# Optimization experiments

Hardware: AMD Instinct MI355X
Metric: run time of the kernel (lower is better)

## Reference

```python
import jax, jax.numpy as jnp
import numpy as np
import math

N_HEADS = 16
D_Q = 1024
D_K = 1024
D_V = 1024
D_OUT = 1024
HID = D_OUT // N_HEADS  # 64
BATCH = 2
SEQ = 2048


def setup_inputs() -> dict:
    key = jax.random.key(0)
    ks = jax.random.split(key, 7)
    stdv = 1.0 / math.sqrt(HID)
    so = 1.0 / math.sqrt(D_OUT)
    return {
        "q": jax.random.normal(ks[0], (BATCH, SEQ, D_Q), dtype=jnp.float32),
        "k": jax.random.normal(ks[1], (BATCH, SEQ, D_K), dtype=jnp.float32),
        "v": jax.random.normal(ks[2], (BATCH, SEQ, D_V), dtype=jnp.float32),
        "W_query": jax.random.uniform(ks[3], (N_HEADS, D_Q, HID), jnp.float32, -stdv, stdv),
        "W_key": jax.random.uniform(ks[4], (N_HEADS, D_K, HID), jnp.float32, -stdv, stdv),
        "W_val": jax.random.uniform(ks[5], (N_HEADS, D_V, HID), jnp.float32, -stdv, stdv),
        "W_out": jax.random.uniform(ks[6], (N_HEADS, HID, D_OUT), jnp.float32, -so, so),
    }


def reference(q, k, v, W_query, W_key, W_val, W_out):
    norm = 1.0 / math.sqrt(HID)
    # per-head projections: [h, b, s, e]
    Q = jnp.einsum("bqd,hde->hbqe", q, W_query)
    K = jnp.einsum("bkd,hde->hbke", k, W_key)
    V = jnp.einsum("bkd,hde->hbke", v, W_val)
    # scaled dot-product attention
    compat = norm * jnp.einsum("hbqe,hbke->hbqk", Q, K)
    attn = jax.nn.softmax(compat, axis=-1)
    heads = jnp.einsum("hbqk,hbke->hbqe", attn, V)
    # output projection: concat heads then W_out == sum over h of per-head proj
    out = jnp.einsum("hbqe,heo->bqo", heads, W_out)
    return out
```

## Files before the change

### kernel.cpp

```cpp
#include <hip/hip_runtime.h>
#include <hip/hip_bf16.h>

typedef __bf16 bf16;
typedef __bf16 bf16x8 __attribute__((ext_vector_type(8)));
typedef __bf16 bf16x4 __attribute__((ext_vector_type(4)));
typedef float  f32x4  __attribute__((ext_vector_type(4)));

#define MFMA16(a,b,c) __builtin_amdgcn_mfma_f32_16x16x32_bf16(a, b, c, 0, 0, 0)

__device__ __forceinline__ void gl2lds16(const bf16* g, bf16* l) {
    __builtin_amdgcn_global_load_lds(
        (__attribute__((address_space(1))) void*)g,
        (__attribute__((address_space(3))) void*)l, 16, 0, 0);
}

__global__ __launch_bounds__(256)
void prep_kernel(const float* __restrict__ q, const float* __restrict__ k,
                 const float* __restrict__ v, const float* __restrict__ Wq,
                 const float* __restrict__ Wk, const float* __restrict__ Wv,
                 const float* __restrict__ Wo, bf16* __restrict__ Xcat,
                 bf16* __restrict__ Wqkv, bf16* __restrict__ Wot)
{
    __shared__ bf16 Tl[64][72];
    const int bid = blockIdx.x;
    const int tid = threadIdx.x;

    if (bid < 6144) {
        int gidx = bid * 256 + tid;
        int t    = gidx >> 19;
        int off  = (gidx & 0x7FFFF) * 8;
        const float* src = (t == 0) ? q : (t == 1) ? k : v;
        const float4 f0 = *(const float4*)&src[off];
        const float4 f1 = *(const float4*)&src[off + 4];
        bf16x8 p = { (bf16)f0.x, (bf16)f0.y, (bf16)f0.z, (bf16)f0.w,
                     (bf16)f1.x, (bf16)f1.y, (bf16)f1.z, (bf16)f1.w };
        *(bf16x8*)&Xcat[(size_t)gidx * 8] = p;
        return;
    }
    if (bid < 6912) {
        int idx = bid - 6144;
        int x = idx & 15, z = idx >> 4;
        int t = z >> 4, h = z & 15;
        const float* inp = ((t == 0) ? Wq : (t == 1) ? Wk : Wv) + (size_t)h * 65536;
        bf16* outp = Wqkv + (size_t)t * 1024 * 1024 + (size_t)h * 65536;
        int r0 = x * 64;
        #pragma unroll
        for (int i = 0; i < 2; i++) {
            int s = tid + i * 256;
            int r = s >> 3, c8 = (s & 7) * 8;
            const float* ap = &inp[(size_t)(r0 + r) * 64 + c8];
            float4 f0 = *(const float4*)ap;
            float4 f1 = *(const float4*)(ap + 4);
            bf16x8 p = { (bf16)f0.x, (bf16)f0.y, (bf16)f0.z, (bf16)f0.w,
                         (bf16)f1.x, (bf16)f1.y, (bf16)f1.z, (bf16)f1.w };
            *(bf16x8*)&Tl[r][c8] = p;
        }
        __syncthreads();
        #pragma unroll
        for (int i = 0; i < 2; i++) {
            int s = tid + i * 256;
            int c = s >> 3, r8 = (s & 7) * 8;
            bf16x8 p;
            #pragma unroll
            for (int j = 0; j < 8; j++) p[j] = Tl[r8 + j][c];
            *(bf16x8*)&outp[(size_t)c * 1024 + r0 + r8] = p;
        }
        return;
    }
    {
        int idx = bid - 6912;
        int y = idx & 15, h = idx >> 4;
        int c0 = y * 64;
        const float* inp = Wo + (size_t)h * 65536;
        bf16* outp = Wot + (size_t)h * 64;
        #pragma unroll
        for (int i = 0; i < 2; i++) {
            int s = tid + i * 256;
            int r = s >> 3, c8 = (s & 7) * 8;
            const float* ap = &inp[(size_t)r * 1024 + c0 + c8];
            float4 f0 = *(const float4*)ap;
            float4 f1 = *(const float4*)(ap + 4);
            bf16x8 p = { (bf16)f0.x, (bf16)f0.y, (bf16)f0.z, (bf16)f0.w,
                         (bf16)f1.x, (bf16)f1.y, (bf16)f1.z, (bf16)f1.w };
            *(bf16x8*)&Tl[r][c8] = p;
        }
        __syncthreads();
        #pragma unroll
        for (int i = 0; i < 2; i++) {
            int s = tid + i * 256;
            int c = s >> 3, r8 = (s & 7) * 8;
            bf16x8 p;
            #pragma unroll
            for (int j = 0; j < 8; j++) p[j] = Tl[r8 + j][c];
            *(bf16x8*)&outp[(size_t)(c0 + c) * 1024 + r8] = p;
        }
    }
}

__global__ __launch_bounds__(256)
void qkv_gemm(const bf16* __restrict__ Xcat, const bf16* __restrict__ Wqkv,
              bf16* __restrict__ Cq, bf16* __restrict__ Ck, bf16* __restrict__ Vt,
              float qscale)
{
    __shared__ bf16 Al[128 * 64];
    __shared__ bf16 Bl[128 * 64];
    const int slab  = blockIdx.x >> 5;
    const int mbase = (blockIdx.x & 31) * 128;
    const int nbase = blockIdx.y * 128;
    const int tid = threadIdx.x;
    const int w = tid >> 6, lane = tid & 63;
    const int lm = lane & 15, q4 = lane >> 4;
    const int wr = (w >> 1) * 64, wc = (w & 1) * 64;
    const int lrow = lane >> 3, lsw = ((lane & 7) ^ lrow) * 8;

    const bf16* A  = Xcat + (size_t)slab * 4096 * 1024;
    const bf16* Bt = Wqkv + (size_t)slab * 1024 * 1024;

    f32x4 acc[4][4] = {};

    for (int k0 = 0; k0 < 1024; k0 += 64) {
        __syncthreads();
        #pragma unroll
        for (int i = 0; i < 4; i++) {
            int c = w * 4 + i;
            gl2lds16(&A [(size_t)(mbase + c * 8 + lrow) * 1024 + k0 + lsw], &Al[c * 512]);
            gl2lds16(&Bt[(size_t)(nbase + c * 8 + lrow) * 1024 + k0 + lsw], &Bl[c * 512]);
        }
        __syncthreads();
        #pragma unroll
        for (int kk2 = 0; kk2 < 2; kk2++) {
            bf16x8 a[4], bfr[4];
            const int g = ((kk2 * 4 + q4) ^ (lm & 7)) * 8;
            #pragma unroll
            for (int i = 0; i < 4; i++) a[i]   = *(const bf16x8*)&Al[(wr + i * 16 + lm) * 64 + g];
            #pragma unroll
            for (int j = 0; j < 4; j++) bfr[j] = *(const bf16x8*)&Bl[(wc + j * 16 + lm) * 64 + g];
            #pragma unroll
            for (int i = 0; i < 4; i++)
                #pragma unroll
                for (int j = 0; j < 4; j++)
                    acc[i][j] = MFMA16(a[i], bfr[j], acc[i][j]);
        }
    }

    if (slab == 2) {
        #pragma unroll
        for (int i = 0; i < 4; i++)
            #pragma unroll
            for (int j = 0; j < 4; j++) {
                int s0  = mbase + wr + i * 16 + q4 * 4;
                int col = nbase + wc + j * 16 + lm;
                int sp  = (s0 & ~31) | (((s0 >> 2) & 3) * 8) | (((s0 >> 4) & 1) * 4);
                bf16x4 p = { (bf16)acc[i][j][0], (bf16)acc[i][j][1],
                             (bf16)acc[i][j][2], (bf16)acc[i][j][3] };
                *(bf16x4*)&Vt[(size_t)col * 4096 + sp] = p;
            }
    } else {
        bf16* C = (slab == 0) ? Cq : Ck;
        const float scale = (slab == 0) ? qscale : 1.0f;
        #pragma unroll
        for (int i = 0; i < 4; i++)
            #pragma unroll
            for (int j = 0; j < 4; j++)
                #pragma unroll
                for (int r = 0; r < 4; r++) {
                    int row = mbase + wr + i * 16 + q4 * 4 + r;
                    int col = nbase + wc + j * 16 + lm;
                    C[(size_t)row * 1024 + col] = (bf16)(acc[i][j][r] * scale);
                }
    }
}

__global__ __launch_bounds__(256)
void outproj_gemm(const bf16* __restrict__ A, const bf16* __restrict__ Bt,
                  float* __restrict__ C)
{
    __shared__ bf16 Al[64 * 64];
    __shared__ bf16 Bl[128 * 64];
    const int mbase = blockIdx.x * 64;
    const int nbase = blockIdx.y * 128;
    const int tid = threadIdx.x;
    const int w = tid >> 6, lane = tid & 63;
    const int lm = lane & 15, q4 = lane >> 4;
    const int wm = (w >> 1) * 32, wn = (w & 1) * 64;
    const int lrow = lane >> 3, lsw = ((lane & 7) ^ lrow) * 8;

    f32x4 acc[2][4] = {};

    for (int k0 = 0; k0 < 1024; k0 += 64) {
        __syncthreads();
        #pragma unroll
        for (int i = 0; i < 2; i++) {
            int c = w * 2 + i;
            gl2lds16(&A[(size_t)(mbase + c * 8 + lrow) * 1024 + k0 + lsw], &Al[c * 512]);
        }
        #pragma unroll
        for (int i = 0; i < 4; i++) {
            int c = w * 4 + i;
            gl2lds16(&Bt[(size_t)(nbase + c * 8 + lrow) * 1024 + k0 + lsw], &Bl[c * 512]);
        }
        __syncthreads();
        #pragma unroll
        for (int kk2 = 0; kk2 < 2; kk2++) {
            bf16x8 a[2], bfr[4];
            const int g = ((kk2 * 4 + q4) ^ (lm & 7)) * 8;
            #pragma unroll
            for (int i = 0; i < 2; i++) a[i]   = *(const bf16x8*)&Al[(wm + i * 16 + lm) * 64 + g];
            #pragma unroll
            for (int j = 0; j < 4; j++) bfr[j] = *(const bf16x8*)&Bl[(wn + j * 16 + lm) * 64 + g];
            #pragma unroll
            for (int i = 0; i < 2; i++)
                #pragma unroll
                for (int j = 0; j < 4; j++)
                    acc[i][j] = MFMA16(a[i], bfr[j], acc[i][j]);
        }
    }

    #pragma unroll
    for (int i = 0; i < 2; i++)
        #pragma unroll
        for (int j = 0; j < 4; j++)
            #pragma unroll
            for (int r = 0; r < 4; r++) {
                int row = mbase + wm + i * 16 + q4 * 4 + r;
                int col = nbase + wn + j * 16 + lm;
                C[(size_t)row * 1024 + col] = acc[i][j][r];
            }
}

__global__ __launch_bounds__(256)
void attn_kernel(const bf16* __restrict__ Qp, const bf16* __restrict__ Kp,
                 const bf16* __restrict__ Vt, bf16* __restrict__ Hd)
{
    __shared__ bf16 Kl[2][64 * 64];
    __shared__ bf16 Vl[2][64 * 64];

    const int qt = blockIdx.x, b = blockIdx.y, h = blockIdx.z;
    const int qbase = qt * 128;
    const int tid  = threadIdx.x;
    const int w    = tid >> 6, lane = tid & 63;
    const int lm   = lane & 15, q4 = lane >> 4;
    const int lrow = lane >> 3, lsw = ((lane & 7) ^ lrow) * 8;

    const bf16* Qh = Qp + (size_t)(b * 2048 + qbase + w * 32) * 1024 + h * 64;
    const bf16* Kh = Kp + (size_t)(b * 2048) * 1024 + h * 64;
    const bf16* Vh = Vt + (size_t)(h * 64) * 4096 + b * 2048;

    bf16x8 Qf[2][2];
    #pragma unroll
    for (int i = 0; i < 2; i++)
        #pragma unroll
        for (int kk2 = 0; kk2 < 2; kk2++)
            Qf[i][kk2] = *(const bf16x8*)&Qh[(size_t)(i * 16 + lm) * 1024 + kk2 * 32 + q4 * 8];

    f32x4 O[2][4] = {};
    float lsum[2] = {};

    auto stage = [&](int kt, int d) {
        #pragma unroll
        for (int i = 0; i < 2; i++) {
            int c = w * 2 + i;
            gl2lds16(&Kh[(size_t)(kt * 64 + c * 8 + lrow) * 1024 + lsw], &Kl[d][c * 512]);
            gl2lds16(&Vh[(size_t)(c * 8 + lrow) * 4096 + kt * 64 + lsw], &Vl[d][c * 512]);
        }
    };

    stage(0, 0);

    for (int kt = 0; kt < 32; kt++) {
        __syncthreads();
        if (kt < 31) stage(kt + 1, (kt + 1) & 1);
        const bf16* Kd = &Kl[kt & 1][0];
        const bf16* Vd = &Vl[kt & 1][0];

        f32x4 St[2][4] = {};
        #pragma unroll
        for (int ctp = 0; ctp < 4; ctp++) {
            #pragma unroll
            for (int kk2 = 0; kk2 < 2; kk2++) {
                const int g = ((kk2 * 4 + q4) ^ (lm & 7)) * 8;
                bf16x8 kf = *(const bf16x8*)&Kd[(ctp * 16 + lm) * 64 + g];
                #pragma unroll
                for (int i = 0; i < 2; i++)
                    St[i][ctp] = MFMA16(kf, Qf[i][kk2], St[i][ctp]);
            }
        }

        #pragma unroll
        for (int kk4 = 0; kk4 < 2; kk4++) {
            bf16x8 Pf[2];
            #pragma unroll
            for (int i = 0; i < 2; i++)
                #pragma unroll
                for (int j = 0; j < 8; j++) {
                    float p = __builtin_amdgcn_exp2f(St[i][kk4 * 2 + (j >> 2)][j & 3]);
                    lsum[i] += p;
                    Pf[i][j] = (bf16)p;
                }
            #pragma unroll
            for (int et = 0; et < 4; et++) {
                const int g = ((kk4 * 4 + q4) ^ (lm & 7)) * 8;
                bf16x8 vf = *(const bf16x8*)&Vd[(et * 16 + lm) * 64 + g];
                #pragma unroll
                for (int i = 0; i < 2; i++)
                    O[i][et] = MFMA16(Pf[i], vf, O[i][et]);
            }
        }
    }

    float rl[2][4];
    #pragma unroll
    for (int i = 0; i < 2; i++) {
        float l = lsum[i];
        l += __shfl_xor(l, 16, 64);
        l += __shfl_xor(l, 32, 64);
        #pragma unroll
        for (int r = 0; r < 4; r++) {
            float lr = __shfl(l, (lane & 48) + ((lane >> 4) & 3) * 4 + r, 64);
            rl[i][r] = 1.0f / lr;
        }
    }

    #pragma unroll
    for (int i = 0; i < 2; i++)
        #pragma unroll
        for (int et = 0; et < 4; et++)
            #pragma unroll
            for (int r = 0; r < 4; r++) {
                int row = b * 2048 + qbase + w * 32 + i * 16 + q4 * 4 + r;
                Hd[(size_t)row * 1024 + h * 64 + et * 16 + lm] =
                    (bf16)(O[i][et][r] * rl[i][r]);
            }
}

extern "C" void kernel_launch(void* const* d_in, const int* in_sizes, int n_in,
                              void* d_out, int out_size, void* d_ws, size_t ws_size,
                              hipStream_t stream)
{
    const float* q  = (const float*)d_in[0];
    const float* k  = (const float*)d_in[1];
    const float* v  = (const float*)d_in[2];
    const float* Wq = (const float*)d_in[3];
    const float* Wk = (const float*)d_in[4];
    const float* Wv = (const float*)d_in[5];
    const float* Wo = (const float*)d_in[6];
    float* out = (float*)d_out;

    const size_t Mi = 1024 * 1024;
    bf16* Xcat  = (bf16*)d_ws;
    bf16* Hd    = Xcat;
    bf16* Wqkv  = Xcat + 12 * Mi;
    bf16* Wot   = Xcat + 15 * Mi;
    bf16* Qproj = Xcat + 16 * Mi;
    bf16* Kproj = Xcat + 20 * Mi;
    bf16* Vtb   = (bf16*)d_out;

    const float qscale = 0.125f * 1.4426950408889634f;

    prep_kernel<<<7168, 256, 0, stream>>>(q, k, v, Wq, Wk, Wv, Wo, Xcat, Wqkv, Wot);
    qkv_gemm<<<dim3(96, 8), 256, 0, stream>>>(Xcat, Wqkv, Qproj, Kproj, Vtb, qscale);
    attn_kernel<<<dim3(16, 2, 16), 256, 0, stream>>>(Qproj, Kproj, Vtb, Hd);
    outproj_gemm<<<dim3(64, 8), 256, 0, stream>>>(Hd, Wot, out);
}
```

Baseline: 216.1 us.

## Halve attention query tile, compute row sums via MFMA, add wave priority hints

```diff
diff --git a/kernel.cpp b/kernel.cpp
--- a/kernel.cpp
+++ b/kernel.cpp
@@ -236,25 +236,26 @@
     __shared__ bf16 Vl[2][64 * 64];
 
     const int qt = blockIdx.x, b = blockIdx.y, h = blockIdx.z;
-    const int qbase = qt * 128;
+    const int qbase = qt * 64;
     const int tid  = threadIdx.x;
     const int w    = tid >> 6, lane = tid & 63;
     const int lm   = lane & 15, q4 = lane >> 4;
     const int lrow = lane >> 3, lsw = ((lane & 7) ^ lrow) * 8;
 
-    const bf16* Qh = Qp + (size_t)(b * 2048 + qbase + w * 32) * 1024 + h * 64;
+    const bf16* Qh = Qp + (size_t)(b * 2048 + qbase + w * 16) * 1024 + h * 64;
     const bf16* Kh = Kp + (size_t)(b * 2048) * 1024 + h * 64;
     const bf16* Vh = Vt + (size_t)(h * 64) * 4096 + b * 2048;
 
-    bf16x8 Qf[2][2];
+    bf16x8 Qf[2];
     #pragma unroll
-    for (int i = 0; i < 2; i++)
-        #pragma unroll
-        for (int kk2 = 0; kk2 < 2; kk2++)
-            Qf[i][kk2] = *(const bf16x8*)&Qh[(size_t)(i * 16 + lm) * 1024 + kk2 * 32 + q4 * 8];
-
-    f32x4 O[2][4] = {};
-    float lsum[2] = {};
+    for (int kk2 = 0; kk2 < 2; kk2++)
+        Qf[kk2] = *(const bf16x8*)&Qh[(size_t)lm * 1024 + kk2 * 32 + q4 * 8];
+
+    const bf16 one = (bf16)1.0f;
+    const bf16x8 ones = { one, one, one, one, one, one, one, one };
+
+    f32x4 O[4] = {};
+    f32x4 Lacc = {};
 
     auto stage = [&](int kt, int d) {
         #pragma unroll
@@ -273,64 +274,49 @@
         const bf16* Kd = &Kl[kt & 1][0];
         const bf16* Vd = &Vl[kt & 1][0];
 
-        f32x4 St[2][4] = {};
+        f32x4 St[4] = {};
+        __builtin_amdgcn_s_setprio(1);
         #pragma unroll
         for (int ctp = 0; ctp < 4; ctp++) {
             #pragma unroll
             for (int kk2 = 0; kk2 < 2; kk2++) {
                 const int g = ((kk2 * 4 + q4) ^ (lm & 7)) * 8;
                 bf16x8 kf = *(const bf16x8*)&Kd[(ctp * 16 + lm) * 64 + g];
-                #pragma unroll
-                for (int i = 0; i < 2; i++)
-                    St[i][ctp] = MFMA16(kf, Qf[i][kk2], St[i][ctp]);
+                St[ctp] = MFMA16(kf, Qf[kk2], St[ctp]);
             }
         }
+        __builtin_amdgcn_s_setprio(0);
 
         #pragma unroll
         for (int kk4 = 0; kk4 < 2; kk4++) {
-            bf16x8 Pf[2];
-            #pragma unroll
-            for (int i = 0; i < 2; i++)
-                #pragma unroll
-                for (int j = 0; j < 8; j++) {
-                    float p = __builtin_amdgcn_exp2f(St[i][kk4 * 2 + (j >> 2)][j & 3]);
-                    lsum[i] += p;
-                    Pf[i][j] = (bf16)p;
-                }
+            bf16x8 Pf;
+            #pragma unroll
+            for (int j = 0; j < 8; j++)
+                Pf[j] = (bf16)__builtin_amdgcn_exp2f(St[kk4 * 2 + (j >> 2)][j & 3]);
+            __builtin_amdgcn_s_setprio(1);
+            Lacc = MFMA16(Pf, ones, Lacc);
             #pragma unroll
             for (int et = 0; et < 4; et++) {
                 const int g = ((kk4 * 4 + q4) ^ (lm & 7)) * 8;
                 bf16x8 vf = *(const bf16x8*)&Vd[(et * 16 + lm) * 64 + g];
-                #pragma unroll
-                for (int i = 0; i < 2; i++)
-                    O[i][et] = MFMA16(Pf[i], vf, O[i][et]);
+                O[et] = MFMA16(Pf, vf, O[et]);
             }
-        }
-    }
-
-    float rl[2][4];
+            __builtin_amdgcn_s_setprio(0);
+        }
+    }
+
+    float rl[4];
     #pragma unroll
-    for (int i = 0; i < 2; i++) {
-        float l = lsum[i];
-        l += __shfl_xor(l, 16, 64);
-        l += __shfl_xor(l, 32, 64);
+    for (int r = 0; r < 4; r++) rl[r] = 1.0f / Lacc[r];
+
+    #pragma unroll
+    for (int et = 0; et < 4; et++)
         #pragma unroll
         for (int r = 0; r < 4; r++) {
-            float lr = __shfl(l, (lane & 48) + ((lane >> 4) & 3) * 4 + r, 64);
-            rl[i][r] = 1.0f / lr;
-        }
-    }
-
-    #pragma unroll
-    for (int i = 0; i < 2; i++)
-        #pragma unroll
-        for (int et = 0; et < 4; et++)
-            #pragma unroll
-            for (int r = 0; r < 4; r++) {
-                int row = b * 2048 + qbase + w * 32 + i * 16 + q4 * 4 + r;
-                Hd[(size_t)row * 1024 + h * 64 + et * 16 + lm] =
-                    (bf16)(O[i][et][r] * rl[i][r]);
-            }
+            int row = b * 2048 + qbase + w * 16 + q4 * 4 + r;
+            Hd[(size_t)row * 1024 + h * 64 + et * 16 + lm] =
+                (bf16)(O[et][r] * rl[r]);
+        }
 }
 
 extern "C" void kernel_launch(void* const* d_in, const int* in_sizes, int n_in,
@@ -359,6 +345,6 @@
 
     prep_kernel<<<7168, 256, 0, stream>>>(q, k, v, Wq, Wk, Wv, Wo, Xcat, Wqkv, Wot);
     qkv_gemm<<<dim3(96, 8), 256, 0, stream>>>(Xcat, Wqkv, Qproj, Kproj, Vtb, qscale);
-    attn_kernel<<<dim3(16, 2, 16), 256, 0, stream>>>(Qproj, Kproj, Vtb, Hd);
+    attn_kernel<<<dim3(32, 2, 16), 256, 0, stream>>>(Qproj, Kproj, Vtb, Hd);
     outproj_gemm<<<dim3(64, 8), 256, 0, stream>>>(Hd, Wot, out);
 }
```

After: 220.5 us. 2.0% more time.

## Split attention KV tiles across warp pairs and double grid size

Applied to the files above, without the earlier changes.

```diff
diff --git a/kernel.cpp b/kernel.cpp
--- a/kernel.cpp
+++ b/kernel.cpp
@@ -228,7 +228,7 @@
             }
 }
 
-__global__ __launch_bounds__(256)
+__global__ __launch_bounds__(256, 4)
 void attn_kernel(const bf16* __restrict__ Qp, const bf16* __restrict__ Kp,
                  const bf16* __restrict__ Vt, bf16* __restrict__ Hd)
 {
@@ -236,13 +236,15 @@
     __shared__ bf16 Vl[2][64 * 64];
 
     const int qt = blockIdx.x, b = blockIdx.y, h = blockIdx.z;
-    const int qbase = qt * 128;
+    const int qbase = qt * 64;
     const int tid  = threadIdx.x;
     const int w    = tid >> 6, lane = tid & 63;
+    const int p    = w & 1;
+    const int kvh  = w >> 1;
     const int lm   = lane & 15, q4 = lane >> 4;
     const int lrow = lane >> 3, lsw = ((lane & 7) ^ lrow) * 8;
 
-    const bf16* Qh = Qp + (size_t)(b * 2048 + qbase + w * 32) * 1024 + h * 64;
+    const bf16* Qh = Qp + (size_t)(b * 2048 + qbase + p * 32) * 1024 + h * 64;
     const bf16* Kh = Kp + (size_t)(b * 2048) * 1024 + h * 64;
     const bf16* Vh = Vt + (size_t)(h * 64) * 4096 + b * 2048;
 
@@ -253,8 +255,11 @@
         for (int kk2 = 0; kk2 < 2; kk2++)
             Qf[i][kk2] = *(const bf16x8*)&Qh[(size_t)(i * 16 + lm) * 1024 + kk2 * 32 + q4 * 8];
 
+    const bf16 one = (bf16)1.0f;
+    const bf16x8 ones = { one, one, one, one, one, one, one, one };
+
     f32x4 O[2][4] = {};
-    float lsum[2] = {};
+    f32x4 Lacc[2] = {};
 
     auto stage = [&](int kt, int d) {
         #pragma unroll
@@ -265,72 +270,91 @@
         }
     };
 
-    stage(0, 0);
-
-    for (int kt = 0; kt < 32; kt++) {
-        __syncthreads();
-        if (kt < 31) stage(kt + 1, (kt + 1) & 1);
-        const bf16* Kd = &Kl[kt & 1][0];
-        const bf16* Vd = &Vl[kt & 1][0];
-
-        f32x4 St[2][4] = {};
-        #pragma unroll
-        for (int ctp = 0; ctp < 4; ctp++) {
+    const int phase = (qt * 3 + h * 5 + b * 16) & 31;
+
+    stage(phase, 0);
+
+    for (int it = 0; it < 32; it++) {
+        __syncthreads();
+        if (it < 31) stage((it + 1 + phase) & 31, (it + 1) & 1);
+        const bf16* Kd = &Kl[it & 1][0];
+        const bf16* Vd = &Vl[it & 1][0];
+
+        f32x4 St[2][2] = {};
+        __builtin_amdgcn_s_setprio(1);
+        #pragma unroll
+        for (int c2 = 0; c2 < 2; c2++) {
+            const int ctp = kvh * 2 + c2;
             #pragma unroll
             for (int kk2 = 0; kk2 < 2; kk2++) {
                 const int g = ((kk2 * 4 + q4) ^ (lm & 7)) * 8;
                 bf16x8 kf = *(const bf16x8*)&Kd[(ctp * 16 + lm) * 64 + g];
                 #pragma unroll
                 for (int i = 0; i < 2; i++)
-                    St[i][ctp] = MFMA16(kf, Qf[i][kk2], St[i][ctp]);
+                    St[i][c2] = MFMA16(kf, Qf[i][kk2], St[i][c2]);
             }
         }
-
-        #pragma unroll
-        for (int kk4 = 0; kk4 < 2; kk4++) {
-            bf16x8 Pf[2];
+        __builtin_amdgcn_s_setprio(0);
+
+        bf16x8 Pf[2];
+        #pragma unroll
+        for (int i = 0; i < 2; i++)
+            #pragma unroll
+            for (int j = 0; j < 8; j++)
+                Pf[i][j] = (bf16)__builtin_amdgcn_exp2f(St[i][j >> 2][j & 3]);
+
+        __builtin_amdgcn_s_setprio(1);
+        #pragma unroll
+        for (int i = 0; i < 2; i++) Lacc[i] = MFMA16(Pf[i], ones, Lacc[i]);
+        const int gv = ((kvh * 4 + q4) ^ (lm & 7)) * 8;
+        #pragma unroll
+        for (int et = 0; et < 4; et++) {
+            bf16x8 vf = *(const bf16x8*)&Vd[(et * 16 + lm) * 64 + gv];
             #pragma unroll
             for (int i = 0; i < 2; i++)
-                #pragma unroll
-                for (int j = 0; j < 8; j++) {
-                    float p = __builtin_amdgcn_exp2f(St[i][kk4 * 2 + (j >> 2)][j & 3]);
-                    lsum[i] += p;
-                    Pf[i][j] = (bf16)p;
+                O[i][et] = MFMA16(Pf[i], vf, O[i][et]);
+        }
+        __builtin_amdgcn_s_setprio(0);
+    }
+
+    __syncthreads();
+    float* Ol = (float*)&Kl[0][0];
+    float* Ll = (float*)&Vl[0][0];
+    if (kvh == 1) {
+        #pragma unroll
+        for (int i = 0; i < 2; i++)
+            #pragma unroll
+            for (int et = 0; et < 4; et++)
+                #pragma unroll
+                for (int r = 0; r < 4; r++)
+                    Ol[p * 2048 + (i * 16 + q4 * 4 + r) * 64 + et * 16 + lm] = O[i][et][r];
+        if (lm == 0) {
+            #pragma unroll
+            for (int i = 0; i < 2; i++)
+                #pragma unroll
+                for (int r = 0; r < 4; r++)
+                    Ll[p * 32 + i * 16 + q4 * 4 + r] = Lacc[i][r];
+        }
+    }
+    __syncthreads();
+    if (kvh == 0) {
+        #pragma unroll
+        for (int i = 0; i < 2; i++) {
+            float rl[4];
+            #pragma unroll
+            for (int r = 0; r < 4; r++)
+                rl[r] = 1.0f / (Lacc[i][r] + Ll[p * 32 + i * 16 + q4 * 4 + r]);
+            #pragma unroll
+            for (int et = 0; et < 4; et++)
+                #pragma unroll
+                for (int r = 0; r < 4; r++) {
+                    float o = O[i][et][r] +
+                              Ol[p * 2048 + (i * 16 + q4 * 4 + r) * 64 + et * 16 + lm];
+                    int row = b * 2048 + qbase + p * 32 + i * 16 + q4 * 4 + r;
+                    Hd[(size_t)row * 1024 + h * 64 + et * 16 + lm] = (bf16)(o * rl[r]);
                 }
-            #pragma unroll
-            for (int et = 0; et < 4; et++) {
-                const int g = ((kk4 * 4 + q4) ^ (lm & 7)) * 8;
-                bf16x8 vf = *(const bf16x8*)&Vd[(et * 16 + lm) * 64 + g];
-                #pragma unroll
-                for (int i = 0; i < 2; i++)
-                    O[i][et] = MFMA16(Pf[i], vf, O[i][et]);
-            }
-        }
-    }
-
-    float rl[2][4];
-    #pragma unroll
-    for (int i = 0; i < 2; i++) {
-        float l = lsum[i];
-        l += __shfl_xor(l, 16, 64);
-        l += __shfl_xor(l, 32, 64);
-        #pragma unroll
-        for (int r = 0; r < 4; r++) {
-            float lr = __shfl(l, (lane & 48) + ((lane >> 4) & 3) * 4 + r, 64);
-            rl[i][r] = 1.0f / lr;
-        }
-    }
-
-    #pragma unroll
-    for (int i = 0; i < 2; i++)
-        #pragma unroll
-        for (int et = 0; et < 4; et++)
-            #pragma unroll
-            for (int r = 0; r < 4; r++) {
-                int row = b * 2048 + qbase + w * 32 + i * 16 + q4 * 4 + r;
-                Hd[(size_t)row * 1024 + h * 64 + et * 16 + lm] =
-                    (bf16)(O[i][et][r] * rl[i][r]);
-            }
+        }
+    }
 }
 
 extern "C" void kernel_launch(void* const* d_in, const int* in_sizes, int n_in,
@@ -359,6 +383,6 @@
 
     prep_kernel<<<7168, 256, 0, stream>>>(q, k, v, Wq, Wk, Wv, Wo, Xcat, Wqkv, Wot);
     qkv_gemm<<<dim3(96, 8), 256, 0, stream>>>(Xcat, Wqkv, Qproj, Kproj, Vtb, qscale);
-    attn_kernel<<<dim3(16, 2, 16), 256, 0, stream>>>(Qproj, Kproj, Vtb, Hd);
+    attn_kernel<<<dim3(32, 2, 16), 256, 0, stream>>>(Qproj, Kproj, Vtb, Hd);
     outproj_gemm<<<dim3(64, 8), 256, 0, stream>>>(Hd, Wot, out);
 }
```

After: 245.5 us. 13.6% more time.
